# Kernel tuning notes

Measured on AMD Instinct MI355X. Metric: run time of the kernel, lower is better.

## Reference

```python
import jax, jax.numpy as jnp
import numpy as np


def setup_inputs() -> dict:
    key = jax.random.key(0)
    k1, k2, k3 = jax.random.split(key, 3)
    B, T, F = 16, 2048, 64
    he = jax.random.normal(k1, (B, T, F), dtype=jnp.float32)
    scale = 1.0 / np.sqrt(F).astype(np.float32)
    W1 = jax.random.normal(k2, (F, F), dtype=jnp.float32) * scale
    W2 = jax.random.normal(k3, (F, F), dtype=jnp.float32) * scale
    return {"he": he, "W1": W1, "W2": W2, "attention_len": 48}


def reference(he, W1, W2, attention_len):
    # he: [B, T, F] encoder states. For each output step i the original module:
    #   1) unrolls L_i = min(attention_len, max(i,1)) decoder steps starting
    #      from he[:, i, :]:  H_k = sigmoid(H_{k-1} @ W1), Y_k = sigmoid(H_k @ W2)
    #   2) attends Y_1..Y_{L_i} against the encoder window he[:, i-L_i:i, :]
    #      with per-step dot-product scores, softmax over the window, and a
    #      weighted sum of the encoder window.
    # (i=0 degenerates to a single-element softmax -> context = he[:, 0, :].)
    B, T, F = he.shape
    A = attention_len

    def step(H, _):
        H = jax.nn.sigmoid(H @ W1)          # [B, T, F]
        Y = jax.nn.sigmoid(H @ W2)          # [B, T, F]
        return H, Y

    # Decoder outputs for every start position, all A steps: Ys[b, i, t, f]
    _, Ys = jax.lax.scan(step, he, None, length=A)   # [A, B, T, F]
    Ys = jnp.moveaxis(Ys, 0, 2)                      # [B, T, A, F]

    i = jnp.arange(T)[:, None]                       # [T, 1]
    t = jnp.arange(A)[None, :]                       # [1, A]
    L = jnp.minimum(A, jnp.maximum(i, 1))            # window length per step
    j = jnp.clip(i - L + t, 0, T - 1)                # encoder index per (i, t)
    valid = t < L                                    # [T, A]

    gathered = he[:, j, :]                           # [B, T, A, F] windowed encoder
    scores = jnp.einsum('btaf,btaf->bta', Ys, gathered)
    scores = jnp.where(valid[None, :, :], scores, jnp.float32(-1e9))
    w = jax.nn.softmax(scores, axis=-1)              # [B, T, A]
    ctx = jnp.einsum('bta,btaf->btf', w, gathered)   # [B, T, F]
    return ctx
```

## Files before the change

kernel.cpp:

```cpp
#include <hip/hip_runtime.h>

#define B_   16
#define T_   2048
#define F_   64
#define A_   48
#define TOK  64
#define WSTR 68
#define SSTR 49
#define NWIN 111

typedef __attribute__((ext_vector_type(4))) _Float16 half4;
typedef __attribute__((ext_vector_type(2))) _Float16 half2;
typedef __attribute__((ext_vector_type(4))) float    f32x4;

#define LOG2E 1.4426950408889634f

__device__ __forceinline__ float sigp(float c) {
    return __builtin_amdgcn_rcpf(1.0f + __builtin_amdgcn_exp2f(c));
}

__device__ __forceinline__ half2 pk2(float a, float b) {
    return __builtin_bit_cast(half2, __builtin_amdgcn_cvt_pkrtz(a, b));
}

__global__ __launch_bounds__(256)
void ContextBlock_kernel(const float* __restrict__ he,
                         const float* __restrict__ W1,
                         const float* __restrict__ W2,
                         float* __restrict__ out)
{
    __shared__ float sWin[NWIN * WSTR];
    __shared__ float sSc[TOK * SSTR];

    const int tid = threadIdx.x;
    const int b   = blockIdx.x >> 5;
    const int t0  = (blockIdx.x & 31) * TOK;
    const float* __restrict__ heB = he + (size_t)b * T_ * F_;

    for (int i = tid; i < NWIN * 16; i += 256) {
        int row = i >> 4, c4 = (i & 15) * 4;
        int g = t0 - 48 + row;
        if (g >= 0) {
            float4 v = *(const float4*)(heB + (size_t)g * F_ + c4);
            *(float4*)(&sWin[row * WSTR + c4]) = v;
        }
    }

    const int lane = tid & 63;
    const int wv   = tid >> 6;
    const int quad = lane >> 4;
    const int ml   = lane & 15;
    const int tw0  = wv * 16;
    const int tg   = t0 + tw0 + ml;
    const int L    = min(A_, max(tg, 1));

    half4 aW1[4][4], aW2[4][4];
    for (int mo = 0; mo < 4; ++mo)
        for (int kt = 0; kt < 4; ++kt) {
            half4 f1, f2;
#pragma unroll
            for (int j = 0; j < 4; ++j) {
                int k = kt * 16 + quad * 4 + j;
                f1[j] = (_Float16)(-LOG2E * W1[k * F_ + mo * 16 + ml]);
                f2[j] = (_Float16)(-LOG2E * W2[k * F_ + mo * 16 + ml]);
            }
            aW1[mo][kt] = f1; aW2[mo][kt] = f2;
        }

    half4 hb[4];
#pragma unroll
    for (int kt = 0; kt < 4; ++kt) {
        float4 v = *(const float4*)(heB + (size_t)tg * F_ + kt * 16 + quad * 4);
        half4 h;
        h[0] = (_Float16)v.x; h[1] = (_Float16)v.y;
        h[2] = (_Float16)v.z; h[3] = (_Float16)v.w;
        hb[kt] = h;
    }
    __syncthreads();

#pragma unroll 4
    for (int a = 0; a < A_; ++a) {
        f32x4 c1[4];
#pragma unroll
        for (int mo = 0; mo < 4; ++mo) {
            f32x4 z = {0.f, 0.f, 0.f, 0.f};
#pragma unroll
            for (int kt = 0; kt < 4; ++kt)
                z = __builtin_amdgcn_mfma_f32_16x16x16f16(aW1[mo][kt], hb[kt], z, 0, 0, 0);
            c1[mo] = z;
        }
#pragma unroll
        for (int mo = 0; mo < 4; ++mo) {
            half2 lo = pk2(sigp(c1[mo][0]), sigp(c1[mo][1]));
            half2 hi = pk2(sigp(c1[mo][2]), sigp(c1[mo][3]));
            half4 h; h[0] = lo[0]; h[1] = lo[1]; h[2] = hi[0]; h[3] = hi[1];
            hb[mo] = h;
        }
        f32x4 c2[4];
#pragma unroll
        for (int mo = 0; mo < 4; ++mo) {
            f32x4 z = {0.f, 0.f, 0.f, 0.f};
#pragma unroll
            for (int kt = 0; kt < 4; ++kt)
                z = __builtin_amdgcn_mfma_f32_16x16x16f16(aW2[mo][kt], hb[kt], z, 0, 0, 0);
            c2[mo] = z;
        }
        int j = tg - L + a; if (j < 0) j = 0;
        const float* wp = &sWin[(j - t0 + 48) * WSTR];
        float p = 0.f;
#pragma unroll
        for (int mo = 0; mo < 4; ++mo) {
            float4 g = *(const float4*)(wp + mo * 16 + quad * 4);
            p += sigp(c2[mo][0]) * g.x + sigp(c2[mo][1]) * g.y
               + sigp(c2[mo][2]) * g.z + sigp(c2[mo][3]) * g.w;
        }
        p += __shfl_xor(p, 16);
        p += __shfl_xor(p, 32);
        if (quad == 0) sSc[(tw0 + ml) * SSTR + a] = (a < L) ? p : -1e9f;
    }
    __syncthreads();

    {
        int r = tid >> 2, s = tid & 3;
        float sc[12];
#pragma unroll
        for (int i = 0; i < 12; ++i) sc[i] = sSc[r * SSTR + i * 4 + s];
        float m = sc[0];
#pragma unroll
        for (int i = 1; i < 12; ++i) m = fmaxf(m, sc[i]);
        m = fmaxf(m, __shfl_xor(m, 1));
        m = fmaxf(m, __shfl_xor(m, 2));
        float e[12]; float sum = 0.f;
#pragma unroll
        for (int i = 0; i < 12; ++i) { e[i] = __expf(sc[i] - m); sum += e[i]; }
        sum += __shfl_xor(sum, 1);
        sum += __shfl_xor(sum, 2);
        float inv = __builtin_amdgcn_rcpf(sum);
#pragma unroll
        for (int i = 0; i < 12; ++i) sSc[r * SSTR + i * 4 + s] = e[i] * inv;
    }
    __syncthreads();

    {
        int r = tid >> 2, fc = (tid & 3) * 16;
        int tgr = t0 + r;
        int Lr = min(A_, max(tgr, 1));
        float acc[16];
#pragma unroll
        for (int q = 0; q < 16; ++q) acc[q] = 0.f;
        for (int a = 0; a < A_; ++a) {
            float wgt = sSc[r * SSTR + a];
            int j = tgr - Lr + a; if (j < 0) j = 0;
            const float* wp = &sWin[(j - t0 + 48) * WSTR + fc];
#pragma unroll
            for (int q = 0; q < 4; ++q) {
                float4 g = *(const float4*)(wp + q * 4);
                acc[q*4+0] += wgt * g.x; acc[q*4+1] += wgt * g.y;
                acc[q*4+2] += wgt * g.z; acc[q*4+3] += wgt * g.w;
            }
        }
        float* op = out + ((size_t)b * T_ + tgr) * F_ + fc;
#pragma unroll
        for (int q = 0; q < 4; ++q)
            *(float4*)(op + q * 4) = make_float4(acc[q*4], acc[q*4+1], acc[q*4+2], acc[q*4+3]);
    }
}

extern "C" void kernel_launch(void* const* d_in, const int* in_sizes, int n_in,
                              void* d_out, int out_size, void* d_ws, size_t ws_size,
                              hipStream_t stream) {
    const float* he = (const float*)d_in[0];
    const float* W1 = (const float*)d_in[1];
    const float* W2 = (const float*)d_in[2];
    float* out = (float*)d_out;
    dim3 grid(B_ * (T_ / TOK));
    dim3 block(256);
    hipLaunchKernelGGL(ContextBlock_kernel, grid, block, 0, stream, he, W1, W2, out);
}
```

Measured before the change: 126.4 us.

## Compute attention scores with MFMA on fp16 window and specialize interior blocks

Result: slower. 163.5 us (+29.4%).

```diff
diff --git a/kernel.cpp b/kernel.cpp
--- a/kernel.cpp
+++ b/kernel.cpp
@@ -6,6 +6,7 @@
 #define A_   48
 #define TOK  64
 #define WSTR 68
+#define HWS  72
 #define SSTR 49
 #define NWIN 111
 
@@ -18,31 +19,33 @@
 __device__ __forceinline__ float sigp(float c) {
     return __builtin_amdgcn_rcpf(1.0f + __builtin_amdgcn_exp2f(c));
 }
-
 __device__ __forceinline__ half2 pk2(float a, float b) {
     return __builtin_bit_cast(half2, __builtin_amdgcn_cvt_pkrtz(a, b));
 }
 
-__global__ __launch_bounds__(256)
-void ContextBlock_kernel(const float* __restrict__ he,
-                         const float* __restrict__ W1,
-                         const float* __restrict__ W2,
-                         float* __restrict__ out)
+template<bool FIRST>
+__device__ __forceinline__ void run_block(int b, int t0,
+                                          const float* __restrict__ he,
+                                          const float* __restrict__ W1,
+                                          const float* __restrict__ W2,
+                                          float* __restrict__ out)
 {
-    __shared__ float sWin[NWIN * WSTR];
-    __shared__ float sSc[TOK * SSTR];
+    __shared__ float          sWin[NWIN * WSTR];
+    __shared__ _Float16       sWinH[NWIN * HWS];
+    __shared__ float          sSc[TOK * SSTR];
 
     const int tid = threadIdx.x;
-    const int b   = blockIdx.x >> 5;
-    const int t0  = (blockIdx.x & 31) * TOK;
     const float* __restrict__ heB = he + (size_t)b * T_ * F_;
 
     for (int i = tid; i < NWIN * 16; i += 256) {
         int row = i >> 4, c4 = (i & 15) * 4;
         int g = t0 - 48 + row;
-        if (g >= 0) {
+        if (!FIRST || g >= 0) {
             float4 v = *(const float4*)(heB + (size_t)g * F_ + c4);
             *(float4*)(&sWin[row * WSTR + c4]) = v;
+            half2 lo = pk2(v.x, v.y), hi = pk2(v.z, v.w);
+            half4 h; h[0] = lo[0]; h[1] = lo[1]; h[2] = hi[0]; h[3] = hi[1];
+            *(half4*)(&sWinH[row * HWS + c4]) = h;
         }
     }
 
@@ -78,6 +81,12 @@
     }
     __syncthreads();
 
+    const bool amDiag = (quad == (ml >> 2));
+    const bool s0 = (ml & 3) == 0, s1 = (ml & 3) == 1, s2 = (ml & 3) == 2;
+    float* scp = &sSc[(tw0 + ml) * SSTR];
+
+    const _Float16* wrow = &sWinH[(tw0 + ml) * HWS + quad * 4];
+
 #pragma unroll 4
     for (int a = 0; a < A_; ++a) {
         f32x4 c1[4];
@@ -105,18 +114,33 @@
                 z = __builtin_amdgcn_mfma_f32_16x16x16f16(aW2[mo][kt], hb[kt], z, 0, 0, 0);
             c2[mo] = z;
         }
-        int j = tg - L + a; if (j < 0) j = 0;
-        const float* wp = &sWin[(j - t0 + 48) * WSTR];
-        float p = 0.f;
-#pragma unroll
-        for (int mo = 0; mo < 4; ++mo) {
-            float4 g = *(const float4*)(wp + mo * 16 + quad * 4);
-            p += sigp(c2[mo][0]) * g.x + sigp(c2[mo][1]) * g.y
-               + sigp(c2[mo][2]) * g.z + sigp(c2[mo][3]) * g.w;
-        }
-        p += __shfl_xor(p, 16);
-        p += __shfl_xor(p, 32);
-        if (quad == 0) sSc[(tw0 + ml) * SSTR + a] = (a < L) ? p : -1e9f;
+        half4 yh[4];
+#pragma unroll
+        for (int mo = 0; mo < 4; ++mo) {
+            half2 lo = pk2(sigp(c2[mo][0]), sigp(c2[mo][1]));
+            half2 hi = pk2(sigp(c2[mo][2]), sigp(c2[mo][3]));
+            half4 h; h[0] = lo[0]; h[1] = lo[1]; h[2] = hi[0]; h[3] = hi[1];
+            yh[mo] = h;
+        }
+        const _Float16* wp;
+        if (FIRST) {
+            int j = tg - L + a; if (j < 0) j = 0;
+            wp = &sWinH[(j + 48) * HWS + quad * 4];
+        } else {
+            wp = wrow; wrow += HWS;
+        }
+        half4 g0 = *(const half4*)(wp);
+        half4 g1 = *(const half4*)(wp + 16);
+        half4 g2 = *(const half4*)(wp + 32);
+        half4 g3 = *(const half4*)(wp + 48);
+        f32x4 zs = {0.f, 0.f, 0.f, 0.f};
+        zs = __builtin_amdgcn_mfma_f32_16x16x16f16(yh[0], g0, zs, 0, 0, 0);
+        zs = __builtin_amdgcn_mfma_f32_16x16x16f16(yh[1], g1, zs, 0, 0, 0);
+        zs = __builtin_amdgcn_mfma_f32_16x16x16f16(yh[2], g2, zs, 0, 0, 0);
+        zs = __builtin_amdgcn_mfma_f32_16x16x16f16(yh[3], g3, zs, 0, 0, 0);
+        float val = s0 ? zs[0] : (s1 ? zs[1] : (s2 ? zs[2] : zs[3]));
+        if (FIRST) val = (a < L) ? val : -1e9f;
+        if (amDiag) scp[a] = val;
     }
     __syncthreads();
 
@@ -150,7 +174,8 @@
         for (int q = 0; q < 16; ++q) acc[q] = 0.f;
         for (int a = 0; a < A_; ++a) {
             float wgt = sSc[r * SSTR + a];
-            int j = tgr - Lr + a; if (j < 0) j = 0;
+            int j = tgr - Lr + a;
+            if (FIRST) { if (j < 0) j = 0; }
             const float* wp = &sWin[(j - t0 + 48) * WSTR + fc];
 #pragma unroll
             for (int q = 0; q < 4; ++q) {
@@ -164,6 +189,23 @@
         for (int q = 0; q < 4; ++q)
             *(float4*)(op + q * 4) = make_float4(acc[q*4], acc[q*4+1], acc[q*4+2], acc[q*4+3]);
     }
+}
+
+__global__ __launch_bounds__(256)
+void ContextBlock_first(const float* __restrict__ he, const float* __restrict__ W1,
+                        const float* __restrict__ W2, float* __restrict__ out)
+{
+    run_block<true>(blockIdx.x, 0, he, W1, W2, out);
+}
+
+__global__ __launch_bounds__(256)
+void ContextBlock_rest(const float* __restrict__ he, const float* __restrict__ W1,
+                       const float* __restrict__ W2, float* __restrict__ out)
+{
+    int blk = blockIdx.x;
+    int b   = blk / 31;
+    int t0  = ((blk % 31) + 1) * TOK;
+    run_block<false>(b, t0, he, W1, W2, out);
 }
 
 extern "C" void kernel_launch(void* const* d_in, const int* in_sizes, int n_in,
@@ -173,7 +215,6 @@
     const float* W1 = (const float*)d_in[1];
     const float* W2 = (const float*)d_in[2];
     float* out = (float*)d_out;
-    dim3 grid(B_ * (T_ / TOK));
-    dim3 block(256);
-    hipLaunchKernelGGL(ContextBlock_kernel, grid, block, 0, stream, he, W1, W2, out);
-}
+    hipLaunchKernelGGL(ContextBlock_rest,  dim3(B_ * 31), dim3(256), 0, stream, he, W1, W2, out);
+    hipLaunchKernelGGL(ContextBlock_first, dim3(B_),      dim3(256), 0, stream, he, W1, W2, out);
+}
```
